# Kernel optimization log

Measured on AMD Instinct MI355X. Metric: run time of the kernel, lower is better.

The kernel has to match this reference:

```python
import jax, jax.numpy as jnp
import numpy as np

# J1 Bessel function of the first kind, single-precision rational/asymptotic
# approximation (Numerical Recipes / Abramowitz & Stegun 9.4), matching
# scipy.special.j1 to ~1e-7 relative accuracy. Fully on-device, jit-able.

def bessel_j1(x):
    ax = jnp.abs(x)
    small = ax < 8.0

    # |x| < 8: rational approximation in y = x^2
    y = x * x
    num = x * (72362614232.0 + y * (-7895059235.0 + y * (242396853.1
          + y * (-2972611.439 + y * (15704.48260 + y * (-30.16036606))))))
    den = 144725228442.0 + y * (2300535178.0 + y * (18583304.74
          + y * (99447.43394 + y * (376.9991397 + y))))
    small_val = num / den

    # |x| >= 8: asymptotic expansion; guard ax to avoid div-by-zero in the
    # untaken branch under jnp.where
    ax_s = jnp.where(small, 8.0, ax)
    z = 8.0 / ax_s
    yy = z * z
    xx = ax_s - 2.356194491  # ax - 3*pi/4
    p1 = 1.0 + yy * (0.183105e-2 + yy * (-0.3516396496e-4
         + yy * (0.2457520174e-5 + yy * (-0.240337019e-6))))
    p2 = 0.04687499995 + yy * (-0.2002690873e-3 + yy * (0.8449199096e-5
         + yy * (-0.88228987e-6 + yy * 0.105787412e-6)))
    big_val = jnp.sqrt(0.636619772 / ax_s) * (jnp.cos(xx) * p1
              - z * jnp.sin(xx) * p2) * jnp.sign(x)

    return jnp.where(small, small_val, big_val)


def setup_inputs() -> dict:
    key = jax.random.key(0)
    ks = jax.random.split(key, 7)
    B, D_in, H, D_out = 32768, 64, 2048, 64
    s1 = 1.0 / np.sqrt(D_in)
    s2 = 1.0 / np.sqrt(H)
    return {
        "t": jax.random.normal(ks[0], (B, D_in), dtype=jnp.float32),
        "W1": jax.random.normal(ks[1], (D_in, H), dtype=jnp.float32) * s1,
        "b1": jax.random.normal(ks[2], (H,), dtype=jnp.float32) * s1,
        "W2": jax.random.normal(ks[3], (H, H), dtype=jnp.float32) * s2,
        "b2": jax.random.normal(ks[4], (H,), dtype=jnp.float32) * s2,
        "W3": jax.random.normal(ks[5], (H, D_out), dtype=jnp.float32) * s2,
        "b3": jax.random.normal(ks[6], (D_out,), dtype=jnp.float32) * s2,
    }


def reference(t, W1, b1, W2, b2, W3, b3):
    h = bessel_j1(t @ W1 + b1)        # Linear -> J1 Bessel
    h = jnp.sin(h @ W2 + b2)          # Linear -> sin
    return h @ W3 + b3                # Linear
```

## Files before the change

### kernel.cpp

```cpp
#include <hip/hip_runtime.h>
#include <cstdint>
#include <cstddef>

typedef unsigned short u16;
typedef __attribute__((ext_vector_type(8))) __bf16 bf16x8;
typedef __attribute__((ext_vector_type(4))) float f32x4;

#define AS1(p) ((const __attribute__((address_space(1))) void*)(p))
#define AS3(p) ((__attribute__((address_space(3))) void*)(p))


__device__ __forceinline__ u16 f2bf(float f) {
    union { float f; unsigned u; } v; v.f = f;
    unsigned r = v.u + 0x7fffu + ((v.u >> 16) & 1u);
    return (u16)(r >> 16);
}

__device__ __forceinline__ float j1f_approx(float x) {
    float ax = fabsf(x);
    float y = x * x;
    float num = x * (7.2362614232e10f + y * (-7.895059235e9f + y * (2.423968531e8f
              + y * (-2.972611439e6f + y * (1.570448260e4f + y * (-3.016036606e1f))))));
    float den = 1.44725228442e11f + y * (2.300535178e9f + y * (1.858330474e7f
              + y * (9.944743394e4f + y * (3.769991397e2f + y))));
    float r = num / den;
    if (__any(ax >= 8.0f)) {
        float z  = 8.0f / ax;
        float yy = z * z;
        float xx = ax - 2.356194491f;
        float p1 = 1.0f + yy * (0.183105e-2f + yy * (-0.3516396496e-4f
                 + yy * (0.2457520174e-5f + yy * (-0.240337019e-6f))));
        float p2 = 0.04687499995f + yy * (-0.2002690873e-3f + yy * (0.8449199096e-5f
                 + yy * (-0.88228987e-6f + yy * 0.105787412e-6f)));
        float big = sqrtf(0.636619772f / ax) * (__cosf(xx) * p1 - z * __sinf(xx) * p2);
        big = copysignf(big, x);
        if (ax >= 8.0f) r = big;
    }
    return r;
}


__global__ void k_f32_to_bf16(const float* __restrict__ in, u16* __restrict__ out, int n) {
    int i = blockIdx.x * 256 + threadIdx.x;
    if (i < n) out[i] = f2bf(in[i]);
}

__global__ void k_transpose_bf16(const float* __restrict__ in, u16* __restrict__ out,
                                 int K, int N) {
    __shared__ float tile[32][33];
    int n0 = blockIdx.x * 32, k0 = blockIdx.y * 32;
    int tx = threadIdx.x, ty = threadIdx.y;
    #pragma unroll
    for (int i = ty; i < 32; i += 8)
        tile[i][tx] = in[(size_t)(k0 + i) * N + n0 + tx];
    __syncthreads();
    #pragma unroll
    for (int i = ty; i < 32; i += 8)
        out[(size_t)(n0 + i) * K + k0 + tx] = f2bf(tile[tx][i]);
}

__global__ void k_init_out(const float* __restrict__ b3, float* __restrict__ out, int n) {
    int i = blockIdx.x * 256 + threadIdx.x;
    if (i < n) out[i] = b3[i & 63];
}


#define BK 32

template<int BM, int BN, int WTM, int WTN, int EPI>
__global__ __launch_bounds__(256)
void k_gemm_bt(const u16* __restrict__ A, int lda,
               const u16* __restrict__ Bt, int ldb,
               const float* __restrict__ bias,
               void* __restrict__ Cout, int ldc,
               int kstart, int klen)
{
    __shared__ __align__(16) u16 Alds[BM * BK];
    __shared__ __align__(16) u16 Blds[BN * BK];

    const int tid  = threadIdx.x;
    const int lane = tid & 63;
    const int wid  = tid >> 6;
    const int wrow = (wid >> 1) * (WTM * 16);
    const int wcol = (wid & 1) * (WTN * 16);
    const int lr   = lane & 15;
    const int lkb  = (lane >> 4) * 8;

    const int brow = blockIdx.y * BM;
    const int bcol = blockIdx.x * BN;
    const int k0 = kstart + blockIdx.z * klen;
    const int k1 = k0 + klen;

    f32x4 acc[WTM][WTN] = {};

    for (int kk = k0; kk < k1; kk += BK) {
        #pragma unroll
        for (int c = tid; c < BM * 4; c += 256) {
            const u16* g = A + (size_t)(brow + (c >> 2)) * lda + kk + (c & 3) * 8;
            __builtin_amdgcn_global_load_lds(AS1(g), AS3(&Alds[c * 8]), 16, 0, 0);
        }
        #pragma unroll
        for (int c = tid; c < BN * 4; c += 256) {
            const u16* g = Bt + (size_t)(bcol + (c >> 2)) * ldb + kk + (c & 3) * 8;
            __builtin_amdgcn_global_load_lds(AS1(g), AS3(&Blds[c * 8]), 16, 0, 0);
        }
        __syncthreads();

        bf16x8 af[WTM], bfr[WTN];
        #pragma unroll
        for (int m = 0; m < WTM; ++m)
            af[m] = *(const bf16x8*)&Alds[(wrow + m * 16 + lr) * BK + lkb];
        #pragma unroll
        for (int n = 0; n < WTN; ++n)
            bfr[n] = *(const bf16x8*)&Blds[(wcol + n * 16 + lr) * BK + lkb];
        #pragma unroll
        for (int m = 0; m < WTM; ++m)
            #pragma unroll
            for (int n = 0; n < WTN; ++n)
                acc[m][n] = __builtin_amdgcn_mfma_f32_16x16x32_bf16(
                                af[m], bfr[n], acc[m][n], 0, 0, 0);
        __syncthreads();
    }

    const int rbase = brow + wrow + (lane >> 4) * 4;
    const int cbase = bcol + wcol + lr;
    #pragma unroll
    for (int n = 0; n < WTN; ++n) {
        const int col = cbase + n * 16;
        float bv = 0.0f;
        if constexpr (EPI != 2) bv = bias[col];
        #pragma unroll
        for (int m = 0; m < WTM; ++m) {
            #pragma unroll
            for (int r = 0; r < 4; ++r) {
                const int row = rbase + m * 16 + r;
                float v = acc[m][n][r];
                if constexpr (EPI == 0) {
                    ((u16*)Cout)[(size_t)row * ldc + col] = f2bf(j1f_approx(v + bv));
                } else {
                    atomicAdd(&((float*)Cout)[(size_t)row * ldc + col], v);
                }
            }
        }
    }
}


__global__ __launch_bounds__(512, 2)
void k_gemm256(const u16* __restrict__ A, int lda,
               const u16* __restrict__ Bt, int ldb,
               const float* __restrict__ bias,
               u16* __restrict__ C, int ldc, int K)
{
    __shared__ __align__(16) u16 lds[65536];

    const int tid  = threadIdx.x;
    const int lane = tid & 63;
    const int wid  = tid >> 6;
    const int wr   = wid >> 2;
    const int wc   = wid & 3;
    const int lr   = lane & 15;
    const int kq   = lane >> 4;

    const int nwg  = gridDim.x * gridDim.y;
    const int bid0 = blockIdx.y * gridDim.x + blockIdx.x;
    const int wg   = (bid0 & 7) * (nwg >> 3) + (bid0 >> 3);
    const int bx   = wg % gridDim.x;
    const int by   = wg / gridDim.x;
    const int brow = by * 256;
    const int bcol = bx * 256;

    const int nT = K >> 6;

    const int srow = tid >> 3;
    const int swz  = (((tid & 7) ^ (srow & 7)) << 3);
    const u16* pgA0 = A  + (size_t)(brow +       srow) * lda + swz;
    const u16* pgA1 = A  + (size_t)(brow + 128 + srow) * lda + swz;
    const u16* pgB0 = Bt + (size_t)(bcol +       srow) * ldb + swz;
    const u16* pgB1 = Bt + (size_t)(bcol + 128 + srow) * ldb + swz;

    auto stg = [&](const u16* base, int ldg, int tile, u16* l0) {
        __builtin_amdgcn_global_load_lds(AS1(base + tile * 64),
                                         AS3(l0 + tid * 8), 16, 0, 0);
        __builtin_amdgcn_global_load_lds(AS1(base + (size_t)64 * ldg + tile * 64),
                                         AS3(l0 + 4096 + tid * 8), 16, 0, 0);
    };

    int a_off[8][2], b_off[4][2];
    #pragma unroll
    for (int m = 0; m < 8; ++m) {
        const int row = m * 16 + lr;
        #pragma unroll
        for (int ks = 0; ks < 2; ++ks)
            a_off[m][ks] = row * 64 + ((ks * 32 + kq * 8) ^ ((row & 7) << 3));
    }
    #pragma unroll
    for (int n = 0; n < 4; ++n) {
        const int row = (wc & 1) * 64 + n * 16 + lr;
        #pragma unroll
        for (int ks = 0; ks < 2; ++ks)
            b_off[n][ks] = row * 64 + ((ks * 32 + kq * 8) ^ ((row & 7) << 3));
    }

    f32x4 acc[8][4] = {};
    bf16x8 af[4][2], bf0[2][2], bf1[2][2];

#define RD_A(mh) { _Pragma("unroll") for (int m = 0; m < 4; ++m) \
                   _Pragma("unroll") for (int ks = 0; ks < 2; ++ks) \
                       af[m][ks] = *(const bf16x8*)&la[a_off[(mh)*4 + m][ks]]; }
#define RD_B0()  { _Pragma("unroll") for (int j = 0; j < 2; ++j) \
                   _Pragma("unroll") for (int ks = 0; ks < 2; ++ks) \
                       bf0[j][ks] = *(const bf16x8*)&lb_[b_off[j][ks]]; }
#define RD_B1()  { _Pragma("unroll") for (int j = 0; j < 2; ++j) \
                   _Pragma("unroll") for (int ks = 0; ks < 2; ++ks) \
                       bf1[j][ks] = *(const bf16x8*)&lb_[b_off[2 + j][ks]]; }
#define MMA(mh, nh, BF) { __builtin_amdgcn_s_setprio(1); \
                      _Pragma("unroll") for (int m = 0; m < 4; ++m) \
                      _Pragma("unroll") for (int j = 0; j < 2; ++j) \
                      _Pragma("unroll") for (int ks = 0; ks < 2; ++ks) \
                          acc[(mh)*4 + m][(nh)*2 + j] = \
                              __builtin_amdgcn_mfma_f32_16x16x32_bf16( \
                                  af[m][ks], BF[j][ks], acc[(mh)*4 + m][(nh)*2 + j], 0, 0, 0); \
                      __builtin_amdgcn_s_setprio(0); }
#define BARRIER()  asm volatile("s_barrier" ::: "memory")
#define SCHED0()   __builtin_amdgcn_sched_barrier(0)

    stg(pgA0, lda, 0, &lds[0]);
    stg(pgA1, lda, 0, &lds[8192]);
    stg(pgB0, ldb, 0, &lds[32768]);
    stg(pgB1, ldb, 0, &lds[32768 + 8192]);
    if (nT > 1) {
        stg(pgA0, lda, 1, &lds[16384]);
        stg(pgA1, lda, 1, &lds[16384 + 8192]);
        asm volatile("s_waitcnt vmcnt(4)" ::: "memory");
    } else {
        asm volatile("s_waitcnt vmcnt(0)" ::: "memory");
    }
    BARRIER();

    for (int t = 0; t < nT; ++t) {
        const int b = t & 1;
        const u16* la  = &lds[b * 16384 + wr * 8192];
        const u16* lb_ = &lds[32768 + b * 16384 + (wc >> 1) * 8192];
        u16* stA = &lds[b * 16384];
        u16* stB = &lds[32768 + (b ^ 1) * 16384];

        RD_A(0); RD_B0();
        if (t + 1 < nT) stg(pgB0, ldb, t + 1, stB);
        BARRIER(); SCHED0();
        MMA(0, 0, bf0);
        RD_B1();
        BARRIER();

        if (t + 1 < nT) stg(pgB1, ldb, t + 1, stB + 8192);
        BARRIER(); SCHED0();
        MMA(0, 1, bf1);
        RD_A(1);
        BARRIER();

        SCHED0();
        MMA(1, 1, bf1);
        BARRIER();

        if (t + 2 < nT) { stg(pgA0, lda, t + 2, stA); stg(pgA1, lda, t + 2, stA + 8192); }
        BARRIER(); SCHED0();
        MMA(1, 0, bf0);
        if (t < nT - 2)       { asm volatile("s_waitcnt vmcnt(4)" ::: "memory"); }
        else if (t == nT - 2) { asm volatile("s_waitcnt vmcnt(0)" ::: "memory"); }
        BARRIER();
    }

#undef RD_A
#undef RD_B0
#undef RD_B1
#undef MMA
#undef BARRIER
#undef SCHED0

    float bv[4];
    #pragma unroll
    for (int n = 0; n < 4; ++n) bv[n] = bias[bcol + wc * 64 + n * 16 + lr];
    #pragma unroll
    for (int m = 0; m < 8; ++m) {
        const int row = brow + wr * 128 + m * 16 + kq * 4;
        #pragma unroll
        for (int n = 0; n < 4; ++n) {
            const int col = bcol + wc * 64 + n * 16 + lr;
            #pragma unroll
            for (int r = 0; r < 4; ++r)
                C[(size_t)(row + r) * ldc + col] = f2bf(__sinf(acc[m][n][r] + bv[n]));
        }
    }
}


extern "C" void kernel_launch(void* const* d_in, const int* in_sizes, int n_in,
                              void* d_out, int out_size, void* d_ws, size_t ws_size,
                              hipStream_t stream) {
    const float* t  = (const float*)d_in[0];
    const float* W1 = (const float*)d_in[1];
    const float* b1 = (const float*)d_in[2];
    const float* W2 = (const float*)d_in[3];
    const float* b2 = (const float*)d_in[4];
    const float* W3 = (const float*)d_in[5];
    const float* b3 = (const float*)d_in[6];
    float* out = (float*)d_out;

    constexpr int B = 32768, Din = 64, H = 2048, Dout = 64;

    char* p = (char*)d_ws;
    u16* t_bf = (u16*)p; p += (size_t)B * Din * 2;
    u16* w1t  = (u16*)p; p += (size_t)H * Din * 2;
    u16* w2t  = (u16*)p; p += (size_t)H * H * 2;
    u16* w3t  = (u16*)p; p += (size_t)Dout * H * 2;
    size_t fixed = (size_t)(p - (char*)d_ws);

    int R = B;
    while (R > 512 && fixed + (size_t)2 * R * H * 2 > ws_size) R >>= 1;
    u16* h1 = (u16*)p;
    u16* h2 = (u16*)(p + (size_t)R * H * 2);

    k_f32_to_bf16<<<(B * Din + 255) / 256, 256, 0, stream>>>(t, t_bf, B * Din);
    k_transpose_bf16<<<dim3(H / 32, Din / 32), dim3(32, 8), 0, stream>>>(W1, w1t, Din, H);
    k_transpose_bf16<<<dim3(H / 32, H / 32), dim3(32, 8), 0, stream>>>(W2, w2t, H, H);
    k_transpose_bf16<<<dim3(Dout / 32, H / 32), dim3(32, 8), 0, stream>>>(W3, w3t, H, Dout);
    k_init_out<<<(out_size + 255) / 256, 256, 0, stream>>>(b3, out, out_size);

    const int SPLITS = 4;
    for (int c0 = 0; c0 < B; c0 += R) {
        const u16* tA = t_bf + (size_t)c0 * Din;
        k_gemm_bt<128, 128, 4, 4, 0><<<dim3(H / 128, R / 128), 256, 0, stream>>>(
            tA, Din, w1t, Din, b1, h1, H, 0, Din);
        k_gemm256<<<dim3(H / 256, R / 256), 512, 0, stream>>>(
            h1, H, w2t, H, b2, h2, H, H);
        k_gemm_bt<128, 64, 4, 2, 2><<<dim3(1, R / 128, SPLITS), 256, 0, stream>>>(
            h2, H, w3t, H, nullptr, out + (size_t)c0 * Dout, Dout, 0, H / SPLITS);
    }
}
```

Baseline: 388.2 us.

## Double-buffer A fragments and cut barriers in the GEMM main loop

Adds a second register buffer for A fragments so both A halves can be read from LDS early, and collapses the eight barriers per k-iteration into two. Sched barriers are removed and replaced by a single lgkmcnt wait before the barrier that guards overwriting the A tile. The aim is less workgroup synchronization and better overlap of LDS reads with MFMA. In exchange it raises register pressure and leaves instruction placement to the compiler's scheduler.

```diff
diff --git a/kernel.cpp b/kernel.cpp
--- a/kernel.cpp
+++ b/kernel.cpp
@@ -203,27 +203,27 @@
     }
 
     f32x4 acc[8][4] = {};
-    bf16x8 af[4][2], bf0[2][2], bf1[2][2];
-
-#define RD_A(mh) { _Pragma("unroll") for (int m = 0; m < 4; ++m) \
+    bf16x8 af0[4][2], af1[4][2], bf0[2][2], bf1[2][2];
+
+#define RD_A(mh, AF) { _Pragma("unroll") for (int m = 0; m < 4; ++m) \
                    _Pragma("unroll") for (int ks = 0; ks < 2; ++ks) \
-                       af[m][ks] = *(const bf16x8*)&la[a_off[(mh)*4 + m][ks]]; }
+                       AF[m][ks] = *(const bf16x8*)&la[a_off[(mh)*4 + m][ks]]; }
 #define RD_B0()  { _Pragma("unroll") for (int j = 0; j < 2; ++j) \
                    _Pragma("unroll") for (int ks = 0; ks < 2; ++ks) \
                        bf0[j][ks] = *(const bf16x8*)&lb_[b_off[j][ks]]; }
 #define RD_B1()  { _Pragma("unroll") for (int j = 0; j < 2; ++j) \
                    _Pragma("unroll") for (int ks = 0; ks < 2; ++ks) \
                        bf1[j][ks] = *(const bf16x8*)&lb_[b_off[2 + j][ks]]; }
-#define MMA(mh, nh, BF) { __builtin_amdgcn_s_setprio(1); \
+#define MMA(mh, nh, AF, BF) { __builtin_amdgcn_s_setprio(1); \
                       _Pragma("unroll") for (int m = 0; m < 4; ++m) \
                       _Pragma("unroll") for (int j = 0; j < 2; ++j) \
                       _Pragma("unroll") for (int ks = 0; ks < 2; ++ks) \
                           acc[(mh)*4 + m][(nh)*2 + j] = \
                               __builtin_amdgcn_mfma_f32_16x16x32_bf16( \
-                                  af[m][ks], BF[j][ks], acc[(mh)*4 + m][(nh)*2 + j], 0, 0, 0); \
+                                  AF[m][ks], BF[j][ks], acc[(mh)*4 + m][(nh)*2 + j], 0, 0, 0); \
                       __builtin_amdgcn_s_setprio(0); }
 #define BARRIER()  asm volatile("s_barrier" ::: "memory")
-#define SCHED0()   __builtin_amdgcn_sched_barrier(0)
+#define LGKM0()    asm volatile("s_waitcnt lgkmcnt(0)" ::: "memory")
 
     stg(pgA0, lda, 0, &lds[0]);
     stg(pgA1, lda, 0, &lds[8192]);
@@ -245,26 +245,20 @@
         u16* stA = &lds[b * 16384];
         u16* stB = &lds[32768 + (b ^ 1) * 16384];
 
-        RD_A(0); RD_B0();
+        RD_A(0, af0); RD_B0();
         if (t + 1 < nT) stg(pgB0, ldb, t + 1, stB);
-        BARRIER(); SCHED0();
-        MMA(0, 0, bf0);
-        RD_B1();
+        MMA(0, 0, af0, bf0);
+        RD_B1(); RD_A(1, af1);
+        if (t + 1 < nT) stg(pgB1, ldb, t + 1, stB + 8192);
+        MMA(0, 1, af0, bf1);
+
+        LGKM0();
         BARRIER();
 
-        if (t + 1 < nT) stg(pgB1, ldb, t + 1, stB + 8192);
-        BARRIER(); SCHED0();
-        MMA(0, 1, bf1);
-        RD_A(1);
-        BARRIER();
-
-        SCHED0();
-        MMA(1, 1, bf1);
-        BARRIER();
-
         if (t + 2 < nT) { stg(pgA0, lda, t + 2, stA); stg(pgA1, lda, t + 2, stA + 8192); }
-        BARRIER(); SCHED0();
-        MMA(1, 0, bf0);
+        MMA(1, 1, af1, bf1);
+        MMA(1, 0, af1, bf0);
+
         if (t < nT - 2)       { asm volatile("s_waitcnt vmcnt(4)" ::: "memory"); }
         else if (t == nT - 2) { asm volatile("s_waitcnt vmcnt(0)" ::: "memory"); }
         BARRIER();
@@ -275,7 +269,7 @@
 #undef RD_B1
 #undef MMA
 #undef BARRIER
-#undef SCHED0
+#undef LGKM0
 
     float bv[4];
     #pragma unroll
```

New measurement: 379.1 us. -2.3%, faster.
